# Optimization experiments

Measured on AMD Instinct MI355X. Metric: run time of the kernel, lower is better.

The kernel has to match this reference:

```python
import jax, jax.numpy as jnp
import numpy as np

N = 8192
IN_DIM, HID_DIM, OUT_DIM = 32, 64, 16


def setup_inputs() -> dict:
    key = jax.random.key(0)
    k1, k2, k3, k4, k5, k6, k7 = jax.random.split(key, 7)
    s1 = 1.0 / np.sqrt(IN_DIM)
    s2 = 1.0 / np.sqrt(HID_DIM)
    return {
        "adj1": jax.random.normal(k1, (N, N), jnp.float32),
        "adj2": jax.random.normal(k2, (N, N), jnp.float32),
        "features": jax.random.normal(k3, (N, IN_DIM), jnp.float32),
        # gc1 linear (shared across both aggregation branches)
        "W1": jax.random.uniform(k4, (IN_DIM, HID_DIM), jnp.float32, -s1, s1),
        "b1": jax.random.uniform(k5, (HID_DIM,), jnp.float32, -s1, s1),
        # gc2 linear
        "W2": jax.random.uniform(k6, (HID_DIM, OUT_DIM), jnp.float32, -s2, s2),
        "b2": jax.random.uniform(k7, (OUT_DIM,), jnp.float32, -s2, s2),
    }


def _gc_layer(adj1, adj2, x, W, b):
    # branch 1: aggregate -> shared linear -> relu
    o1 = jax.nn.relu(jnp.matmul(adj1, x) @ W + b)
    # branch 2: same linear weights
    o2 = jax.nn.relu(jnp.matmul(adj2, x) @ W + b)
    return o1 + o2


def reference(adj1, adj2, features, W1, b1, W2, b2):
    h1 = _gc_layer(adj1, adj2, features, W1, b1)  # [N, HID_DIM]
    h2 = _gc_layer(adj1, adj2, h1, W2, b2)        # [N, OUT_DIM]
    return h2
```

## Files before the change

### kernel.cpp

```cpp
#include <hip/hip_runtime.h>
#include <stdint.h>

#define NN 8192
#define IN_DIM 32
#define HID_DIM 64
#define OUT_DIM 16

typedef __attribute__((ext_vector_type(8))) short short8;
typedef __attribute__((ext_vector_type(4))) float f32x4;

__device__ __forceinline__ short f2bf_bits(float x){
  uint32_t u = __builtin_bit_cast(uint32_t, x);
  u += 0x7FFFu + ((u >> 16) & 1u);
  return (short)(u >> 16);
}

__device__ __forceinline__ short8 cvt8(f32x4 lo, f32x4 hi){
  short8 r;
  r[0]=f2bf_bits(lo[0]); r[1]=f2bf_bits(lo[1]); r[2]=f2bf_bits(lo[2]); r[3]=f2bf_bits(lo[3]);
  r[4]=f2bf_bits(hi[0]); r[5]=f2bf_bits(hi[1]); r[6]=f2bf_bits(hi[2]); r[7]=f2bf_bits(hi[3]);
  return r;
}

__global__ __launch_bounds__(256) void k_g(const float* __restrict__ X, const float* __restrict__ W1,
                                           short* __restrict__ Gt){
  const int b    = blockIdx.x;
  const int rb   = (b & 127) * 64;
  const int cg   = b >> 7;
  const int lane = threadIdx.x & 63;
  const int c    = cg * 4 + (threadIdx.x >> 6);
  const int r    = rb + lane;
  const float* xr = X + (size_t)r * IN_DIM;
  float acc = 0.f;
  #pragma unroll
  for (int k = 0; k < IN_DIM; ++k)
    acc += xr[k] * W1[(size_t)k * HID_DIM + c];
  Gt[(size_t)c * NN + r] = f2bf_bits(acc);
}

template<int REV>
__global__ __launch_bounds__(256) void mm_lds(const float* __restrict__ adj1, const float* __restrict__ adj2,
                                              const short* __restrict__ Bt,
                                              float* __restrict__ P1, float* __restrict__ P2, int klen){
  __shared__ __align__(16) float sA1[64 * 128];
  __shared__ __align__(16) float sA2[64 * 128];
  const int tid  = threadIdx.x;
  const int lane = tid & 63;
  const int wave = tid >> 6;
  const int bm   = REV ? ((int)gridDim.x - 1 - (int)blockIdx.x) : (int)blockIdx.x;
  const int ks   = REV ? ((int)gridDim.y - 1 - (int)blockIdx.y) : (int)blockIdx.y;
  const int k0   = ks * klen;
  const int ngrp = klen >> 7;

  const int srow = tid >> 5;
  const int sgg  = (tid & 31) ^ (srow & 7);
  const size_t grow_base = (size_t)(bm * 64) * NN;

  const int rl = wave * 16 + (lane & 15);
  const int sw = lane & 7;
  const int qh = lane >> 4;

  f32x4 acc1[4] = {{0,0,0,0},{0,0,0,0},{0,0,0,0},{0,0,0,0}};
  f32x4 acc2[4] = {{0,0,0,0},{0,0,0,0},{0,0,0,0},{0,0,0,0}};

  #pragma unroll 1
  for (int gi = 0; gi < ngrp; ++gi){
    const int g     = REV ? (ngrp - 1 - gi) : gi;
    const int kbase = k0 + g * 128;

    if (gi) __syncthreads();

    {
      const size_t colb = (size_t)kbase + (size_t)sgg * 4;
      #pragma unroll
      for (int p = 0; p < 8; ++p){
        const float* s1 = adj1 + grow_base + (size_t)(p * 8 + srow) * NN + colb;
        const float* s2 = adj2 + grow_base + (size_t)(p * 8 + srow) * NN + colb;
        __builtin_amdgcn_global_load_lds(
            (const __attribute__((address_space(1))) void*)s1,
            (__attribute__((address_space(3))) void*)&sA1[p * 1024 + tid * 4], 16, 0, 0);
        __builtin_amdgcn_global_load_lds(
            (const __attribute__((address_space(1))) void*)s2,
            (__attribute__((address_space(3))) void*)&sA2[p * 1024 + tid * 4], 16, 0, 0);
      }
    }
    __syncthreads();

    #pragma unroll
    for (int j = 0; j < 4; ++j){
      const int gr0 = j * 8 + qh * 2;
      const int o0  = rl * 128 + ((gr0     ^ sw) << 2);
      const int o1  = rl * 128 + (((gr0+1) ^ sw) << 2);
      f32x4 lo1 = *(const f32x4*)&sA1[o0];
      f32x4 hi1 = *(const f32x4*)&sA1[o1];
      f32x4 lo2 = *(const f32x4*)&sA2[o0];
      f32x4 hi2 = *(const f32x4*)&sA2[o1];
      short8 b[4];
      const size_t bk = (size_t)kbase + j * 32 + qh * 8;
      #pragma unroll
      for (int f = 0; f < 4; ++f)
        b[f] = *(const short8*)(Bt + (size_t)(f * 16 + (lane & 15)) * NN + bk);
      short8 fa1 = cvt8(lo1, hi1);
      short8 fa2 = cvt8(lo2, hi2);
      #pragma unroll
      for (int f = 0; f < 4; ++f){
        acc1[f] = __builtin_amdgcn_mfma_f32_16x16x32_bf16(fa1, b[f], acc1[f], 0, 0, 0);
        acc2[f] = __builtin_amdgcn_mfma_f32_16x16x32_bf16(fa2, b[f], acc2[f], 0, 0, 0);
      }
    }
  }

  const int orow = bm * 64 + wave * 16 + qh * 4;
  const int col  = lane & 15;
  float* p1 = P1 + ((size_t)ks * NN + orow) * HID_DIM + col;
  float* p2 = P2 + ((size_t)ks * NN + orow) * HID_DIM + col;
  #pragma unroll
  for (int r = 0; r < 4; ++r){
    #pragma unroll
    for (int f = 0; f < 4; ++f){
      p1[(size_t)r * HID_DIM + f * 16] = acc1[f][r];
      p2[(size_t)r * HID_DIM + f * 16] = acc2[f][r];
    }
  }
}

__global__ __launch_bounds__(256) void l1_combine(const float* __restrict__ Y1p, const float* __restrict__ Y2p,
                                                  const float* __restrict__ b1,
                                                  short* __restrict__ H1t, int S){
  const int lane = threadIdx.x & 63;
  const int wave = threadIdx.x >> 6;
  const int row  = blockIdx.x * 4 + wave;
  float s1 = 0.f, s2 = 0.f;
  for (int sp = 0; sp < S; ++sp){
    s1 += Y1p[((size_t)sp * NN + row) * HID_DIM + lane];
    s2 += Y2p[((size_t)sp * NN + row) * HID_DIM + lane];
  }
  const float b = b1[lane];
  float h = fmaxf(s1 + b, 0.f) + fmaxf(s2 + b, 0.f);
  H1t[(size_t)lane * NN + row] = f2bf_bits(h);
}

__global__ __launch_bounds__(256) void l2_combine(const float* __restrict__ Z1p, const float* __restrict__ Z2p,
                                                  const float* __restrict__ W2, const float* __restrict__ b2,
                                                  float* __restrict__ out, int S){
  __shared__ float sW[HID_DIM * OUT_DIM];
  __shared__ float sb[OUT_DIM];
  __shared__ float sz[4][2][HID_DIM];
  const int tid = threadIdx.x;
  for (int i = tid; i < HID_DIM * OUT_DIM; i += 256) sW[i] = W2[i];
  if (tid < OUT_DIM) sb[tid] = b2[tid];
  const int sub = tid >> 6, t = tid & 63;
  const int row = blockIdx.x * 4 + sub;
  float s1 = 0.f, s2 = 0.f;
  for (int sp = 0; sp < S; ++sp){
    s1 += Z1p[((size_t)sp * NN + row) * HID_DIM + t];
    s2 += Z2p[((size_t)sp * NN + row) * HID_DIM + t];
  }
  sz[sub][0][t] = s1;
  sz[sub][1][t] = s2;
  __syncthreads();
  if (t < OUT_DIM){
    float a = sb[t], b = sb[t];
    #pragma unroll
    for (int k = 0; k < HID_DIM; ++k){
      a += sz[sub][0][k] * sW[k * OUT_DIM + t];
      b += sz[sub][1][k] * sW[k * OUT_DIM + t];
    }
    out[(size_t)row * OUT_DIM + t] = fmaxf(a, 0.f) + fmaxf(b, 0.f);
  }
}

extern "C" void kernel_launch(void* const* d_in, const int* in_sizes, int n_in,
                              void* d_out, int out_size, void* d_ws, size_t ws_size,
                              hipStream_t stream){
  const float* adj1 = (const float*)d_in[0];
  const float* adj2 = (const float*)d_in[1];
  const float* X    = (const float*)d_in[2];
  const float* W1   = (const float*)d_in[3];
  const float* b1   = (const float*)d_in[4];
  const float* W2   = (const float*)d_in[5];
  const float* b2   = (const float*)d_in[6];
  float* out = (float*)d_out;

  char* ws = (char*)d_ws;
  short* Gt  = (short*)ws;
  short* H1t = (short*)(ws + (size_t)1024 * 1024);
  const size_t off = (size_t)2 * 1024 * 1024;

  int S = 4;
  while (S > 1 && off + (size_t)S * 4 * 1024 * 1024 > ws_size) S >>= 1;
  float* P1 = (float*)(ws + off);
  float* P2 = P1 + (size_t)S * NN * HID_DIM;
  const int klen = NN / S;

  k_g        <<<dim3(2048),       dim3(256), 0, stream>>>(X, W1, Gt);
  mm_lds<0>  <<<dim3(NN / 64, S), dim3(256), 0, stream>>>(adj1, adj2, Gt, P1, P2, klen);
  l1_combine <<<dim3(NN / 4),     dim3(256), 0, stream>>>(P1, P2, b1, H1t, S);
  mm_lds<1>  <<<dim3(NN / 64, S), dim3(256), 0, stream>>>(adj1, adj2, H1t, P1, P2, klen);
  l2_combine <<<dim3(NN / 4),     dim3(256), 0, stream>>>(P1, P2, W2, b2, out, S);
}
```

Before: 266.7 us.

## Double-buffer adjacency tiles in matmul and coalesce H1 transpose via LDS

Splits the K tile into 64-wide chunks with two LDS buffers so the next chunk's global-to-LDS load is issued before computing on the current one, aiming to overlap memory traffic with MFMA work. The l1_combine kernel now accumulates a 64-row block into LDS and writes the transposed bf16 output with contiguous stores instead of strided ones. The overlap may be limited if the compiler's waitcnt before barriers drains the prefetch early, and smaller tiles add more barriers.

```diff
diff --git a/kernel.cpp b/kernel.cpp
--- a/kernel.cpp
+++ b/kernel.cpp
@@ -39,22 +39,21 @@
 }
 
 template<int REV>
-__global__ __launch_bounds__(256) void mm_lds(const float* __restrict__ adj1, const float* __restrict__ adj2,
-                                              const short* __restrict__ Bt,
-                                              float* __restrict__ P1, float* __restrict__ P2, int klen){
-  __shared__ __align__(16) float sA1[64 * 128];
-  __shared__ __align__(16) float sA2[64 * 128];
+__global__ __launch_bounds__(256) void mm_db(const float* __restrict__ adj1, const float* __restrict__ adj2,
+                                             const short* __restrict__ Bt,
+                                             float* __restrict__ P1, float* __restrict__ P2, int klen){
+  __shared__ __align__(16) float sA[2][2][64 * 64];
   const int tid  = threadIdx.x;
   const int lane = tid & 63;
   const int wave = tid >> 6;
   const int bm   = REV ? ((int)gridDim.x - 1 - (int)blockIdx.x) : (int)blockIdx.x;
   const int ks   = REV ? ((int)gridDim.y - 1 - (int)blockIdx.y) : (int)blockIdx.y;
   const int k0   = ks * klen;
-  const int ngrp = klen >> 7;
-
-  const int srow = tid >> 5;
-  const int sgg  = (tid & 31) ^ (srow & 7);
-  const size_t grow_base = (size_t)(bm * 64) * NN;
+  const int ngrp = klen >> 6;
+
+  const int srow = tid >> 4;
+  const int sg   = (tid & 15) ^ (srow & 7);
+  const size_t growb = (size_t)(bm * 64) * NN;
 
   const int rl = wave * 16 + (lane & 15);
   const int sw = lane & 7;
@@ -63,38 +62,42 @@
   f32x4 acc1[4] = {{0,0,0,0},{0,0,0,0},{0,0,0,0},{0,0,0,0}};
   f32x4 acc2[4] = {{0,0,0,0},{0,0,0,0},{0,0,0,0},{0,0,0,0}};
 
+  auto stage = [&](int t){
+    const int g     = REV ? (ngrp - 1 - t) : t;
+    const int buf   = t & 1;
+    const size_t colb = (size_t)(k0 + g * 64) + (size_t)sg * 4;
+    #pragma unroll
+    for (int p = 0; p < 4; ++p){
+      const float* s1 = adj1 + growb + (size_t)(p * 16 + srow) * NN + colb;
+      const float* s2 = adj2 + growb + (size_t)(p * 16 + srow) * NN + colb;
+      __builtin_amdgcn_global_load_lds(
+          (const __attribute__((address_space(1))) void*)s1,
+          (__attribute__((address_space(3))) void*)&sA[buf][0][p * 1024 + tid * 4], 16, 0, 0);
+      __builtin_amdgcn_global_load_lds(
+          (const __attribute__((address_space(1))) void*)s2,
+          (__attribute__((address_space(3))) void*)&sA[buf][1][p * 1024 + tid * 4], 16, 0, 0);
+    }
+  };
+
+  stage(0);
+  __syncthreads();
+
   #pragma unroll 1
   for (int gi = 0; gi < ngrp; ++gi){
+    if (gi + 1 < ngrp) stage(gi + 1);
+
     const int g     = REV ? (ngrp - 1 - gi) : gi;
-    const int kbase = k0 + g * 128;
-
-    if (gi) __syncthreads();
-
-    {
-      const size_t colb = (size_t)kbase + (size_t)sgg * 4;
-      #pragma unroll
-      for (int p = 0; p < 8; ++p){
-        const float* s1 = adj1 + grow_base + (size_t)(p * 8 + srow) * NN + colb;
-        const float* s2 = adj2 + grow_base + (size_t)(p * 8 + srow) * NN + colb;
-        __builtin_amdgcn_global_load_lds(
-            (const __attribute__((address_space(1))) void*)s1,
-            (__attribute__((address_space(3))) void*)&sA1[p * 1024 + tid * 4], 16, 0, 0);
-        __builtin_amdgcn_global_load_lds(
-            (const __attribute__((address_space(1))) void*)s2,
-            (__attribute__((address_space(3))) void*)&sA2[p * 1024 + tid * 4], 16, 0, 0);
-      }
-    }
-    __syncthreads();
-
-    #pragma unroll
-    for (int j = 0; j < 4; ++j){
+    const int buf   = gi & 1;
+    const int kbase = k0 + g * 64;
+    #pragma unroll
+    for (int j = 0; j < 2; ++j){
       const int gr0 = j * 8 + qh * 2;
-      const int o0  = rl * 128 + ((gr0     ^ sw) << 2);
-      const int o1  = rl * 128 + (((gr0+1) ^ sw) << 2);
-      f32x4 lo1 = *(const f32x4*)&sA1[o0];
-      f32x4 hi1 = *(const f32x4*)&sA1[o1];
-      f32x4 lo2 = *(const f32x4*)&sA2[o0];
-      f32x4 hi2 = *(const f32x4*)&sA2[o1];
+      const int o0  = rl * 64 + ((gr0     ^ sw) << 2);
+      const int o1  = rl * 64 + (((gr0+1) ^ sw) << 2);
+      f32x4 lo1 = *(const f32x4*)&sA[buf][0][o0];
+      f32x4 hi1 = *(const f32x4*)&sA[buf][0][o1];
+      f32x4 lo2 = *(const f32x4*)&sA[buf][1][o0];
+      f32x4 hi2 = *(const f32x4*)&sA[buf][1][o1];
       short8 b[4];
       const size_t bk = (size_t)kbase + j * 32 + qh * 8;
       #pragma unroll
@@ -108,6 +111,7 @@
         acc2[f] = __builtin_amdgcn_mfma_f32_16x16x32_bf16(fa2, b[f], acc2[f], 0, 0, 0);
       }
     }
+    __syncthreads();
   }
 
   const int orow = bm * 64 + wave * 16 + qh * 4;
@@ -127,17 +131,27 @@
 __global__ __launch_bounds__(256) void l1_combine(const float* __restrict__ Y1p, const float* __restrict__ Y2p,
                                                   const float* __restrict__ b1,
                                                   short* __restrict__ H1t, int S){
-  const int lane = threadIdx.x & 63;
-  const int wave = threadIdx.x >> 6;
-  const int row  = blockIdx.x * 4 + wave;
-  float s1 = 0.f, s2 = 0.f;
-  for (int sp = 0; sp < S; ++sp){
-    s1 += Y1p[((size_t)sp * NN + row) * HID_DIM + lane];
-    s2 += Y2p[((size_t)sp * NN + row) * HID_DIM + lane];
-  }
-  const float b = b1[lane];
-  float h = fmaxf(s1 + b, 0.f) + fmaxf(s2 + b, 0.f);
-  H1t[(size_t)lane * NN + row] = f2bf_bits(h);
+  __shared__ float sH[64][65];
+  const int tid = threadIdx.x, lane = tid & 63, wave = tid >> 6;
+  const int rb = blockIdx.x * 64;
+  const float bc = b1[lane];
+  #pragma unroll 4
+  for (int rq = 0; rq < 16; ++rq){
+    const int r = rq * 4 + wave;
+    const int row = rb + r;
+    float s1 = 0.f, s2 = 0.f;
+    for (int sp = 0; sp < S; ++sp){
+      s1 += Y1p[((size_t)sp * NN + row) * HID_DIM + lane];
+      s2 += Y2p[((size_t)sp * NN + row) * HID_DIM + lane];
+    }
+    sH[r][lane] = fmaxf(s1 + bc, 0.f) + fmaxf(s2 + bc, 0.f);
+  }
+  __syncthreads();
+  #pragma unroll 4
+  for (int i = 0; i < 16; ++i){
+    const int c = wave * 16 + i;
+    H1t[(size_t)c * NN + rb + lane] = f2bf_bits(sH[lane][c]);
+  }
 }
 
 __global__ __launch_bounds__(256) void l2_combine(const float* __restrict__ Z1p, const float* __restrict__ Z2p,
@@ -194,8 +208,8 @@
   const int klen = NN / S;
 
   k_g        <<<dim3(2048),       dim3(256), 0, stream>>>(X, W1, Gt);
-  mm_lds<0>  <<<dim3(NN / 64, S), dim3(256), 0, stream>>>(adj1, adj2, Gt, P1, P2, klen);
-  l1_combine <<<dim3(NN / 4),     dim3(256), 0, stream>>>(P1, P2, b1, H1t, S);
-  mm_lds<1>  <<<dim3(NN / 64, S), dim3(256), 0, stream>>>(adj1, adj2, H1t, P1, P2, klen);
+  mm_db<0>   <<<dim3(NN / 64, S), dim3(256), 0, stream>>>(adj1, adj2, Gt, P1, P2, klen);
+  l1_combine <<<dim3(NN / 64),    dim3(256), 0, stream>>>(P1, P2, b1, H1t, S);
+  mm_db<1>   <<<dim3(NN / 64, S), dim3(256), 0, stream>>>(adj1, adj2, H1t, P1, P2, klen);
   l2_combine <<<dim3(NN / 4),     dim3(256), 0, stream>>>(P1, P2, W2, b2, out, S);
 }
```

Result: faster. 260.8 us (-2.2%).
